# Kernel optimization log

Measured on AMD Instinct MI355X. Metric: run time of the kernel, lower is better.

## Reference

```python
import jax, jax.numpy as jnp
import numpy as np

N, E, HID, HEADS, C, G = 50000, 800000, 64, 4, 64, 64
NEG_SLOPE = 0.2

def _p(key, shape, scale=0.05):
    return jax.random.normal(key, shape, dtype=jnp.float32) * scale

def setup_inputs() -> dict:
    key = jax.random.key(0)
    ks = jax.random.split(key, 24)
    inp = {
        "x": jax.random.normal(ks[0], (N, 6), dtype=jnp.float32),
        "node_type": jax.random.randint(ks[1], (N,), 0, 3, dtype=jnp.int32),
        "edge_index": jax.random.randint(ks[2], (2, E), 0, N, dtype=jnp.int32),
        "edge_attr": jax.random.normal(ks[3], (E, 11), dtype=jnp.float32),
        "batch": jnp.sort(jax.random.randint(ks[4], (N,), 0, G, dtype=jnp.int32)),
        "global_feats": jax.random.normal(ks[5], (G, 6), dtype=jnp.float32),
        # parameters
        "type_emb": _p(ks[6], (3, 4), 1.0),
        "enc_W": _p(ks[7], (10, HID)), "enc_b": jnp.zeros((HID,), jnp.float32),
        "Wl": _p(ks[8], (HID, HEADS * C)), "bl": jnp.zeros((HEADS * C,), jnp.float32),
        "Wr": _p(ks[9], (HID, HEADS * C)), "br": jnp.zeros((HEADS * C,), jnp.float32),
        "We": _p(ks[10], (11, HEADS * C)),
        "att": _p(ks[11], (HEADS, C), 0.1),
        "conv_bias": jnp.zeros((HID,), jnp.float32),
        "gW": _p(ks[12], (6, HID)), "gb": jnp.zeros((HID,), jnp.float32),
        "h1W": _p(ks[13], (2 * HID, HID)), "h1b": jnp.zeros((HID,), jnp.float32),
        "h2W": _p(ks[14], (HID, 1)), "h2b": jnp.zeros((1,), jnp.float32),
    }
    return inp

def reference(x, node_type, edge_index, edge_attr, batch, global_feats,
              type_emb, enc_W, enc_b, Wl, bl, Wr, br, We, att, conv_bias,
              gW, gb, h1W, h1b, h2W, h2b):
    n = x.shape[0]
    g = global_feats.shape[0]
    # node encoder: concat type embedding, linear + relu
    h = jax.nn.relu(jnp.concatenate([x, type_emb[node_type]], axis=1) @ enc_W + enc_b)  # [N, HID]
    # add self-loops with fill_value='mean' edge_attr (PyG default)
    src, dst = edge_index[0], edge_index[1]
    cnt = jax.ops.segment_sum(jnp.ones((edge_attr.shape[0], 1), edge_attr.dtype), dst, num_segments=n)
    loop_attr = jax.ops.segment_sum(edge_attr, dst, num_segments=n) / jnp.maximum(cnt, 1.0)
    loops = jnp.arange(n, dtype=src.dtype)
    src = jnp.concatenate([src, loops]); dst = jnp.concatenate([dst, loops])
    ea = jnp.concatenate([edge_attr, loop_attr], axis=0)  # [E+N, 11]
    # GATv2 transforms
    xl = (h @ Wl + bl).reshape(n, HEADS, C)  # source transform
    xr = (h @ Wr + br).reshape(n, HEADS, C)  # target transform
    ee = (ea @ We).reshape(-1, HEADS, C)     # edge transform
    m = jax.nn.leaky_relu(xl[src] + xr[dst] + ee, NEG_SLOPE)  # [E+N, HEADS, C]
    logits = jnp.einsum('ehc,hc->eh', m, att)  # [E+N, HEADS]
    # segment softmax over incoming edges per target node
    lmax = jax.ops.segment_max(logits, dst, num_segments=n)
    alpha = jnp.exp(logits - lmax[dst])
    denom = jax.ops.segment_sum(alpha, dst, num_segments=n)
    alpha = alpha / (denom[dst] + 1e-16)
    out = jax.ops.segment_sum(alpha[:, :, None] * xl[src], dst, num_segments=n)  # [N, HEADS, C]
    hconv = jax.nn.relu(out.mean(axis=1) + conv_bias)  # concat=False -> mean heads
    # global mean pool over graphs
    gcnt = jax.ops.segment_sum(jnp.ones((n, 1), hconv.dtype), batch, num_segments=g)
    pooled = jax.ops.segment_sum(hconv, batch, num_segments=g) / jnp.maximum(gcnt, 1.0)
    gproj = jax.nn.relu(global_feats @ gW + gb)
    combined = jnp.concatenate([pooled, gproj], axis=1)
    outh = jax.nn.relu(combined @ h1W + h1b) @ h2W + h2b  # dropout inactive (eval)
    return outh.squeeze(1)
```

## Files before the change

### kernel.cpp

```cpp
#include <hip/hip_runtime.h>

#define NEG_SLOPE 0.2f

__device__ __forceinline__ float rl(float v, int l) {
    return __uint_as_float(__builtin_amdgcn_readlane(__float_as_uint(v), l));
}

__global__ void k_deg(const int* __restrict__ dst, int* __restrict__ degi, int E) {
    int e = blockIdx.x * blockDim.x + threadIdx.x;
    if (e >= E) return;
    atomicAdd(&degi[dst[e]], 1);
}

__global__ void __launch_bounds__(1024) k_scan(const int* __restrict__ degi,
                                               int* __restrict__ row_ptr,
                                               int* __restrict__ cursor, int N) {
    __shared__ int wsum[16];
    __shared__ int srun;
    int tid = threadIdx.x, lane = tid & 63, wid = tid >> 6;
    if (tid == 0) srun = 0;
    __syncthreads();
    for (int base = 0; base < N; base += 1024) {
        int i = base + tid;
        int v = (i < N) ? degi[i] : 0;
        int x = v;
#pragma unroll
        for (int off = 1; off < 64; off <<= 1) {
            int y = __shfl_up(x, off, 64);
            if (lane >= off) x += y;
        }
        if (lane == 63) wsum[wid] = x;
        __syncthreads();
        if (wid == 0) {
            int w = (lane < 16) ? wsum[lane] : 0;
#pragma unroll
            for (int off = 1; off < 16; off <<= 1) {
                int y = __shfl_up(w, off, 64);
                if (lane >= off) w += y;
            }
            if (lane < 16) wsum[lane] = w;
        }
        __syncthreads();
        int wofs = (wid > 0) ? wsum[wid - 1] : 0;
        int run = srun;
        if (i < N) {
            int ex = run + wofs + x - v;
            row_ptr[i] = ex;
            cursor[i] = ex;
        }
        __syncthreads();
        if (tid == 1023) srun = run + wsum[15];
        __syncthreads();
    }
    if (tid == 0) row_ptr[N] = srun;
}

__global__ void k_fill(const int* __restrict__ src, const int* __restrict__ dst,
                       int* __restrict__ cursor, int2* __restrict__ csr, int E) {
    int e = blockIdx.x * blockDim.x + threadIdx.x;
    if (e >= E) return;
    int d = dst[e];
    int pos = atomicAdd(&cursor[d], 1);
    csr[pos] = make_int2(src[e], e);
}

__global__ void __launch_bounds__(256) k_enc_xlxr(
    const float* __restrict__ x, const int* __restrict__ node_type,
    const float* __restrict__ type_emb,
    const float* __restrict__ enc_W, const float* __restrict__ enc_b,
    const float* __restrict__ Wl, const float* __restrict__ bl,
    const float* __restrict__ Wr, const float* __restrict__ br,
    float* __restrict__ xl, float* __restrict__ xr, int N) {
    const int NPB = 16;
    __shared__ float sIn[NPB][10];
    __shared__ float sH[NPB][64];
    int tid = threadIdx.x;
    int v0 = blockIdx.x * NPB;
    for (int i = tid; i < NPB * 10; i += 256) {
        int v = i / 10, k = i % 10;
        int vg = v0 + v;
        float val = 0.f;
        if (vg < N) {
            if (k < 6) val = x[(size_t)vg * 6 + k];
            else       val = type_emb[node_type[vg] * 4 + (k - 6)];
        }
        sIn[v][k] = val;
    }
    __syncthreads();
    for (int i = tid; i < NPB * 64; i += 256) {
        int v = i >> 6, j = i & 63;
        float acc = enc_b[j];
#pragma unroll
        for (int k = 0; k < 10; ++k) acc += sIn[v][k] * enc_W[k * 64 + j];
        sH[v][j] = fmaxf(acc, 0.f);
    }
    __syncthreads();
    int j = tid;
    float accL[NPB], accR[NPB];
    float blj = bl[j], brj = br[j];
#pragma unroll
    for (int v = 0; v < NPB; ++v) { accL[v] = blj; accR[v] = brj; }
    for (int k = 0; k < 64; ++k) {
        float wl = Wl[k * 256 + j], wr = Wr[k * 256 + j];
#pragma unroll
        for (int v = 0; v < NPB; ++v) {
            float hv = sH[v][k];
            accL[v] += hv * wl;
            accR[v] += hv * wr;
        }
    }
#pragma unroll
    for (int v = 0; v < NPB; ++v) {
        int vg = v0 + v;
        if (vg < N) {
            xl[(size_t)vg * 256 + j] = accL[v];
            xr[(size_t)vg * 256 + j] = accR[v];
        }
    }
}

__global__ void __launch_bounds__(256, 4) k_gather(
    const int2* __restrict__ csr, const float* __restrict__ edge_attr,
    const int* __restrict__ row_ptr, const float* __restrict__ We,
    const float* __restrict__ att, const float* __restrict__ xl,
    const float* __restrict__ xr, const float* __restrict__ conv_bias,
    const int* __restrict__ batch, float* __restrict__ pooled,
    float* __restrict__ gcnt, int N) {
    int tid = threadIdx.x;
    int lane = tid & 63;
    int h = lane >> 4;
    int c16 = lane & 15;
    int colBase = h * 64 + c16 * 4;
    int v = blockIdx.x * 4 + (tid >> 6);
    if (v >= N) return;

    float rWe[11][4];
#pragma unroll
    for (int k = 0; k < 11; ++k) {
        float4 w = *(const float4*)(We + k * 256 + colBase);
        rWe[k][0] = w.x; rWe[k][1] = w.y; rWe[k][2] = w.z; rWe[k][3] = w.w;
    }
    float4 attv = *(const float4*)(att + colBase);
    float4 xrv  = *(const float4*)(xr + (size_t)v * 256 + colBase);

    float acc0 = 0.f, acc1 = 0.f, acc2 = 0.f, acc3 = 0.f, den = 0.f;
    float ea0 = 0.f, ea1 = 0.f, ea2 = 0.f, ea3 = 0.f;

    int rs = row_ptr[v], re = row_ptr[v + 1];
    int deg = re - rs;
    int attrLaneC = lane / 11; if (attrLaneC > 3) attrLaneC = 3;
    int attrLaneK = lane - attrLaneC * 11;

    for (int base = rs; base < re; base += 64) {
        int cnt = re - base; if (cnt > 64) cnt = 64;
        int cm1 = cnt - 1;
        int2 se = csr[base + ((lane < cnt) ? lane : 0)];
        int myS = se.x, myE = se.y;

        auto LOADB = [&](int t0, float& attrR, float4& x0, float4& x1, float4& x2, float4& x3) {
            int ei = t0 + attrLaneC; if (ei > cm1) ei = cm1;
            int eL = __shfl(myE, ei, 64);
            float a = 0.f;
            if (lane < 44) a = edge_attr[(size_t)eL * 11 + attrLaneK];
            attrR = a;
            int i1 = t0 + 1; if (i1 > cm1) i1 = cm1;
            int i2 = t0 + 2; if (i2 > cm1) i2 = cm1;
            int i3 = t0 + 3; if (i3 > cm1) i3 = cm1;
            int s0 = __builtin_amdgcn_readfirstlane(__shfl(myS, t0, 64));
            int s1 = __builtin_amdgcn_readfirstlane(__shfl(myS, i1, 64));
            int s2 = __builtin_amdgcn_readfirstlane(__shfl(myS, i2, 64));
            int s3 = __builtin_amdgcn_readfirstlane(__shfl(myS, i3, 64));
            x0 = *(const float4*)(xl + (size_t)s0 * 256 + colBase);
            x1 = *(const float4*)(xl + (size_t)s1 * 256 + colBase);
            x2 = *(const float4*)(xl + (size_t)s2 * 256 + colBase);
            x3 = *(const float4*)(xl + (size_t)s3 * 256 + colBase);
        };

        auto EDGE = [&](float attrR, float4 xlv, int cbase) {
            float e0 = 0.f, e1 = 0.f, e2 = 0.f, e3 = 0.f;
#pragma unroll
            for (int k = 0; k < 11; ++k) {
                float s = rl(attrR, cbase + k);
                e0 += s * rWe[k][0]; e1 += s * rWe[k][1];
                e2 += s * rWe[k][2]; e3 += s * rWe[k][3];
            }
            ea0 += e0; ea1 += e1; ea2 += e2; ea3 += e3;
            float m0 = xlv.x + xrv.x + e0;
            float m1 = xlv.y + xrv.y + e1;
            float m2 = xlv.z + xrv.z + e2;
            float m3 = xlv.w + xrv.w + e3;
            m0 = (m0 > 0.f) ? m0 : NEG_SLOPE * m0;
            m1 = (m1 > 0.f) ? m1 : NEG_SLOPE * m1;
            m2 = (m2 > 0.f) ? m2 : NEG_SLOPE * m2;
            m3 = (m3 > 0.f) ? m3 : NEG_SLOPE * m3;
            float t2 = m0 * attv.x + m1 * attv.y + m2 * attv.z + m3 * attv.w;
#pragma unroll
            for (int off = 1; off < 16; off <<= 1) t2 += __shfl_xor(t2, off, 64);
            float p = __expf(t2);
            acc0 += p * xlv.x; acc1 += p * xlv.y; acc2 += p * xlv.z; acc3 += p * xlv.w;
            den += p;
        };

        auto PROC = [&](int t0, float attrR, float4 x0, float4 x1, float4 x2, float4 x3) {
            EDGE(attrR, x0, 0);
            if (t0 + 1 < cnt) EDGE(attrR, x1, 11);
            if (t0 + 2 < cnt) EDGE(attrR, x2, 22);
            if (t0 + 3 < cnt) EDGE(attrR, x3, 33);
        };

        int nb = (cnt + 3) >> 2;
        float attrA, attrB;
        float4 xA0, xA1, xA2, xA3, xB0, xB1, xB2, xB3;
        LOADB(0, attrA, xA0, xA1, xA2, xA3);
        int b = 0;
        while (true) {
            if (b + 1 < nb) LOADB((b + 1) * 4, attrB, xB0, xB1, xB2, xB3);
            PROC(b * 4, attrA, xA0, xA1, xA2, xA3);
            ++b; if (b >= nb) break;
            if (b + 1 < nb) LOADB((b + 1) * 4, attrA, xA0, xA1, xA2, xA3);
            PROC(b * 4, attrB, xB0, xB1, xB2, xB3);
            ++b; if (b >= nb) break;
        }
    }

    {
        float inv = 1.f / fmaxf((float)deg, 1.f);
        float4 xself = *(const float4*)(xl + (size_t)v * 256 + colBase);
        float e0 = ea0 * inv, e1 = ea1 * inv, e2 = ea2 * inv, e3 = ea3 * inv;
        float m0 = xself.x + xrv.x + e0;
        float m1 = xself.y + xrv.y + e1;
        float m2 = xself.z + xrv.z + e2;
        float m3 = xself.w + xrv.w + e3;
        m0 = (m0 > 0.f) ? m0 : NEG_SLOPE * m0;
        m1 = (m1 > 0.f) ? m1 : NEG_SLOPE * m1;
        m2 = (m2 > 0.f) ? m2 : NEG_SLOPE * m2;
        m3 = (m3 > 0.f) ? m3 : NEG_SLOPE * m3;
        float t2 = m0 * attv.x + m1 * attv.y + m2 * attv.z + m3 * attv.w;
#pragma unroll
        for (int off = 1; off < 16; off <<= 1) t2 += __shfl_xor(t2, off, 64);
        float p = __expf(t2);
        acc0 += p * xself.x; acc1 += p * xself.y; acc2 += p * xself.z; acc3 += p * xself.w;
        den += p;
    }

    float r = 1.f / (den + 1e-16f);
    float o0 = acc0 * r, o1 = acc1 * r, o2 = acc2 * r, o3 = acc3 * r;
#pragma unroll
    for (int mask = 16; mask <= 32; mask <<= 1) {
        o0 += __shfl_xor(o0, mask, 64);
        o1 += __shfl_xor(o1, mask, 64);
        o2 += __shfl_xor(o2, mask, 64);
        o3 += __shfl_xor(o3, mask, 64);
    }
    int g = batch[v];
    if (lane < 16) {
        float4 cb = *(const float4*)(conv_bias + c16 * 4);
        float* pg = pooled + g * 64 + c16 * 4;
        atomicAdd(&pg[0], fmaxf(0.25f * o0 + cb.x, 0.f));
        atomicAdd(&pg[1], fmaxf(0.25f * o1 + cb.y, 0.f));
        atomicAdd(&pg[2], fmaxf(0.25f * o2 + cb.z, 0.f));
        atomicAdd(&pg[3], fmaxf(0.25f * o3 + cb.w, 0.f));
    }
    if (lane == 0) atomicAdd(&gcnt[g], 1.0f);
}

__global__ void k_final(const float* __restrict__ pooled, const float* __restrict__ gcnt,
                        const float* __restrict__ gf, const float* __restrict__ gW,
                        const float* __restrict__ gb, const float* __restrict__ h1W,
                        const float* __restrict__ h1b, const float* __restrict__ h2W,
                        const float* __restrict__ h2b, float* __restrict__ out, int G) {
    __shared__ float sComb[128];
    __shared__ float sHid[64];
    int g = blockIdx.x;
    int t = threadIdx.x;
    if (t < 64) {
        sComb[t] = pooled[(size_t)g * 64 + t] / fmaxf(gcnt[g], 1.0f);
    } else {
        int j = t - 64;
        float acc = gb[j];
#pragma unroll
        for (int k = 0; k < 6; ++k) acc += gf[(size_t)g * 6 + k] * gW[k * 64 + j];
        sComb[64 + j] = fmaxf(acc, 0.f);
    }
    __syncthreads();
    if (t < 64) {
        float acc = h1b[t];
#pragma unroll
        for (int k = 0; k < 128; ++k) acc += sComb[k] * h1W[k * 64 + t];
        sHid[t] = fmaxf(acc, 0.f);
    }
    __syncthreads();
    if (t < 64) {
        float p = sHid[t] * h2W[t];
#pragma unroll
        for (int off = 32; off > 0; off >>= 1) p += __shfl_xor(p, off, 64);
        if (t == 0) out[g] = p + h2b[0];
    }
}

extern "C" void kernel_launch(void* const* d_in, const int* in_sizes, int n_in,
                              void* d_out, int out_size, void* d_ws, size_t ws_size,
                              hipStream_t stream) {
    const float* x         = (const float*)d_in[0];
    const int*   node_type = (const int*)d_in[1];
    const int*   edge_index= (const int*)d_in[2];
    const float* edge_attr = (const float*)d_in[3];
    const int*   batch     = (const int*)d_in[4];
    const float* gf        = (const float*)d_in[5];
    const float* type_emb  = (const float*)d_in[6];
    const float* enc_W     = (const float*)d_in[7];
    const float* enc_b     = (const float*)d_in[8];
    const float* Wl        = (const float*)d_in[9];
    const float* bl        = (const float*)d_in[10];
    const float* Wr        = (const float*)d_in[11];
    const float* br        = (const float*)d_in[12];
    const float* We        = (const float*)d_in[13];
    const float* att       = (const float*)d_in[14];
    const float* conv_bias = (const float*)d_in[15];
    const float* gW        = (const float*)d_in[16];
    const float* gb        = (const float*)d_in[17];
    const float* h1W       = (const float*)d_in[18];
    const float* h1b       = (const float*)d_in[19];
    const float* h2W       = (const float*)d_in[20];
    const float* h2b       = (const float*)d_in[21];
    float* out = (float*)d_out;

    const int N = in_sizes[0] / 6;
    const int E = in_sizes[2] / 2;
    const int G = in_sizes[5] / 6;

    const int* srcArr = edge_index;
    const int* dstArr = edge_index + E;

    char* wsb = (char*)d_ws;
    size_t off = 0;
    float* xl      = (float*)(wsb + off); off += (size_t)N * 256 * 4;
    float* xr      = (float*)(wsb + off); off += (size_t)N * 256 * 4;
    int2*  csr     = (int2*) (wsb + off); off += (size_t)E * 8;
    int*   row_ptr = (int*)  (wsb + off); off += (size_t)(N + 1) * 4;
    int*   cursor  = (int*)  (wsb + off); off += (size_t)N * 4;
    size_t zs = off;
    int*   degi    = (int*)  (wsb + off); off += (size_t)N * 4;
    float* pooled  = (float*)(wsb + off); off += (size_t)G * 64 * 4;
    float* gcnt    = (float*)(wsb + off); off += (size_t)G * 4;
    size_t ze = off;
    (void)ws_size; (void)n_in; (void)out_size;

    hipMemsetAsync(wsb + zs, 0, ze - zs, stream);

    k_deg<<<(E + 255) / 256, 256, 0, stream>>>(dstArr, degi, E);
    k_enc_xlxr<<<(N + 15) / 16, 256, 0, stream>>>(x, node_type, type_emb, enc_W, enc_b,
                                                  Wl, bl, Wr, br, xl, xr, N);
    k_scan<<<1, 1024, 0, stream>>>(degi, row_ptr, cursor, N);
    k_fill<<<(E + 255) / 256, 256, 0, stream>>>(srcArr, dstArr, cursor, csr, E);
    k_gather<<<(N + 3) / 4, 256, 0, stream>>>(csr, edge_attr, row_ptr, We, att, xl, xr,
                                              conv_bias, batch, pooled, gcnt, N);
    k_final<<<G, 128, 0, stream>>>(pooled, gcnt, gf, gW, gb, h1W, h1b, h2W, h2b, out, G);
}
```

Baseline: 836.8 us.

## Parallelize CSR scan and batch four-edge processing in gather kernel

Replaces the single-block serial prefix scan with a three-kernel multi-block scan (block-local scan, block-sum scan, offset add), which removes a long single-CU serial loop over all nodes. In the gather kernel, the per-edge attention math is restructured so that four edges are processed together: edge-feature projections, leaky-relu logits and the cross-lane reductions are interleaved for ILP, and invalid edges are masked instead of branched on. Source index extraction switches from shfl+readfirstlane to a direct readlane, and the occupancy hint changes to waves_per_eu(3,4). The four-edge batching raises register pressure and does wasted work on partial groups. The scan adds two kernel launches and only supports up to 64 blocks.

```diff
diff --git a/kernel.cpp b/kernel.cpp
--- a/kernel.cpp
+++ b/kernel.cpp
@@ -12,47 +12,58 @@
     atomicAdd(&degi[dst[e]], 1);
 }
 
-__global__ void __launch_bounds__(1024) k_scan(const int* __restrict__ degi,
-                                               int* __restrict__ row_ptr,
-                                               int* __restrict__ cursor, int N) {
+__global__ void __launch_bounds__(1024) k_scan1(const int* __restrict__ degi,
+                                                int* __restrict__ row_ptr,
+                                                int* __restrict__ bsum, int N) {
     __shared__ int wsum[16];
-    __shared__ int srun;
     int tid = threadIdx.x, lane = tid & 63, wid = tid >> 6;
-    if (tid == 0) srun = 0;
-    __syncthreads();
-    for (int base = 0; base < N; base += 1024) {
-        int i = base + tid;
-        int v = (i < N) ? degi[i] : 0;
-        int x = v;
-#pragma unroll
-        for (int off = 1; off < 64; off <<= 1) {
-            int y = __shfl_up(x, off, 64);
-            if (lane >= off) x += y;
-        }
-        if (lane == 63) wsum[wid] = x;
-        __syncthreads();
-        if (wid == 0) {
-            int w = (lane < 16) ? wsum[lane] : 0;
-#pragma unroll
-            for (int off = 1; off < 16; off <<= 1) {
-                int y = __shfl_up(w, off, 64);
-                if (lane >= off) w += y;
-            }
-            if (lane < 16) wsum[lane] = w;
-        }
-        __syncthreads();
-        int wofs = (wid > 0) ? wsum[wid - 1] : 0;
-        int run = srun;
-        if (i < N) {
-            int ex = run + wofs + x - v;
-            row_ptr[i] = ex;
-            cursor[i] = ex;
-        }
-        __syncthreads();
-        if (tid == 1023) srun = run + wsum[15];
-        __syncthreads();
-    }
-    if (tid == 0) row_ptr[N] = srun;
+    int i = blockIdx.x * 1024 + tid;
+    int v = (i < N) ? degi[i] : 0;
+    int x = v;
+#pragma unroll
+    for (int off = 1; off < 64; off <<= 1) {
+        int y = __shfl_up(x, off, 64);
+        if (lane >= off) x += y;
+    }
+    if (lane == 63) wsum[wid] = x;
+    __syncthreads();
+    if (wid == 0) {
+        int w = (lane < 16) ? wsum[lane] : 0;
+#pragma unroll
+        for (int off = 1; off < 16; off <<= 1) {
+            int y = __shfl_up(w, off, 64);
+            if (lane >= off) w += y;
+        }
+        if (lane < 16) wsum[lane] = w;
+    }
+    __syncthreads();
+    int wofs = (wid > 0) ? wsum[wid - 1] : 0;
+    if (i < N) row_ptr[i] = wofs + x - v;
+    if (tid == 0) bsum[blockIdx.x] = wsum[15];
+}
+
+__global__ void k_scan2(int* __restrict__ bsum, int* __restrict__ row_ptr, int nb, int N) {
+    int lane = threadIdx.x & 63;
+    int v = (lane < nb) ? bsum[lane] : 0;
+    int x = v;
+#pragma unroll
+    for (int off = 1; off < 64; off <<= 1) {
+        int y = __shfl_up(x, off, 64);
+        if (lane >= off) x += y;
+    }
+    if (lane < nb) bsum[lane] = x - v;
+    if (lane == 63) row_ptr[N] = x;
+}
+
+__global__ void __launch_bounds__(1024) k_scan3(int* __restrict__ row_ptr,
+                                                int* __restrict__ cursor,
+                                                const int* __restrict__ bsum, int N) {
+    int i = blockIdx.x * 1024 + threadIdx.x;
+    if (i < N) {
+        int r = row_ptr[i] + bsum[blockIdx.x];
+        row_ptr[i] = r;
+        cursor[i] = r;
+    }
 }
 
 __global__ void k_fill(const int* __restrict__ src, const int* __restrict__ dst,
@@ -119,7 +130,8 @@
     }
 }
 
-__global__ void __launch_bounds__(256, 4) k_gather(
+__global__ void __launch_bounds__(256) __attribute__((amdgpu_waves_per_eu(3, 4)))
+k_gather(
     const int2* __restrict__ csr, const float* __restrict__ edge_attr,
     const int* __restrict__ row_ptr, const float* __restrict__ We,
     const float* __restrict__ att, const float* __restrict__ xl,
@@ -166,46 +178,68 @@
             int i1 = t0 + 1; if (i1 > cm1) i1 = cm1;
             int i2 = t0 + 2; if (i2 > cm1) i2 = cm1;
             int i3 = t0 + 3; if (i3 > cm1) i3 = cm1;
-            int s0 = __builtin_amdgcn_readfirstlane(__shfl(myS, t0, 64));
-            int s1 = __builtin_amdgcn_readfirstlane(__shfl(myS, i1, 64));
-            int s2 = __builtin_amdgcn_readfirstlane(__shfl(myS, i2, 64));
-            int s3 = __builtin_amdgcn_readfirstlane(__shfl(myS, i3, 64));
+            int s0 = __builtin_amdgcn_readlane(myS, t0);
+            int s1 = __builtin_amdgcn_readlane(myS, i1);
+            int s2 = __builtin_amdgcn_readlane(myS, i2);
+            int s3 = __builtin_amdgcn_readlane(myS, i3);
             x0 = *(const float4*)(xl + (size_t)s0 * 256 + colBase);
             x1 = *(const float4*)(xl + (size_t)s1 * 256 + colBase);
             x2 = *(const float4*)(xl + (size_t)s2 * 256 + colBase);
             x3 = *(const float4*)(xl + (size_t)s3 * 256 + colBase);
         };
 
-        auto EDGE = [&](float attrR, float4 xlv, int cbase) {
-            float e0 = 0.f, e1 = 0.f, e2 = 0.f, e3 = 0.f;
+        auto PROC4 = [&](int t0, float attrR, float4 x0, float4 x1, float4 x2, float4 x3) {
+            float p00=0.f,p01=0.f,p02=0.f,p03=0.f;
+            float p10=0.f,p11=0.f,p12=0.f,p13=0.f;
+            float p20=0.f,p21=0.f,p22=0.f,p23=0.f;
+            float p30=0.f,p31=0.f,p32=0.f,p33=0.f;
 #pragma unroll
             for (int k = 0; k < 11; ++k) {
-                float s = rl(attrR, cbase + k);
-                e0 += s * rWe[k][0]; e1 += s * rWe[k][1];
-                e2 += s * rWe[k][2]; e3 += s * rWe[k][3];
+                float w0 = rWe[k][0], w1 = rWe[k][1], w2 = rWe[k][2], w3 = rWe[k][3];
+                float s0 = rl(attrR, k), s1 = rl(attrR, 11 + k);
+                float s2 = rl(attrR, 22 + k), s3 = rl(attrR, 33 + k);
+                p00 += s0*w0; p01 += s0*w1; p02 += s0*w2; p03 += s0*w3;
+                p10 += s1*w0; p11 += s1*w1; p12 += s1*w2; p13 += s1*w3;
+                p20 += s2*w0; p21 += s2*w1; p22 += s2*w2; p23 += s2*w3;
+                p30 += s3*w0; p31 += s3*w1; p32 += s3*w2; p33 += s3*w3;
             }
-            ea0 += e0; ea1 += e1; ea2 += e2; ea3 += e3;
-            float m0 = xlv.x + xrv.x + e0;
-            float m1 = xlv.y + xrv.y + e1;
-            float m2 = xlv.z + xrv.z + e2;
-            float m3 = xlv.w + xrv.w + e3;
-            m0 = (m0 > 0.f) ? m0 : NEG_SLOPE * m0;
-            m1 = (m1 > 0.f) ? m1 : NEG_SLOPE * m1;
-            m2 = (m2 > 0.f) ? m2 : NEG_SLOPE * m2;
-            m3 = (m3 > 0.f) ? m3 : NEG_SLOPE * m3;
-            float t2 = m0 * attv.x + m1 * attv.y + m2 * attv.z + m3 * attv.w;
-#pragma unroll
-            for (int off = 1; off < 16; off <<= 1) t2 += __shfl_xor(t2, off, 64);
-            float p = __expf(t2);
-            acc0 += p * xlv.x; acc1 += p * xlv.y; acc2 += p * xlv.z; acc3 += p * xlv.w;
-            den += p;
-        };
-
-        auto PROC = [&](int t0, float attrR, float4 x0, float4 x1, float4 x2, float4 x3) {
-            EDGE(attrR, x0, 0);
-            if (t0 + 1 < cnt) EDGE(attrR, x1, 11);
-            if (t0 + 2 < cnt) EDGE(attrR, x2, 22);
-            if (t0 + 3 < cnt) EDGE(attrR, x3, 33);
+            bool v1 = (t0 + 1 < cnt), v2 = (t0 + 2 < cnt), v3 = (t0 + 3 < cnt);
+            ea0 += p00 + (v1 ? p10 : 0.f) + (v2 ? p20 : 0.f) + (v3 ? p30 : 0.f);
+            ea1 += p01 + (v1 ? p11 : 0.f) + (v2 ? p21 : 0.f) + (v3 ? p31 : 0.f);
+            ea2 += p02 + (v1 ? p12 : 0.f) + (v2 ? p22 : 0.f) + (v3 ? p32 : 0.f);
+            ea3 += p03 + (v1 ? p13 : 0.f) + (v2 ? p23 : 0.f) + (v3 ? p33 : 0.f);
+            float m, t20, t21, t22, t23;
+            m = x0.x+xrv.x+p00; m=(m>0.f)?m:NEG_SLOPE*m; t20  = m*attv.x;
+            m = x0.y+xrv.y+p01; m=(m>0.f)?m:NEG_SLOPE*m; t20 += m*attv.y;
+            m = x0.z+xrv.z+p02; m=(m>0.f)?m:NEG_SLOPE*m; t20 += m*attv.z;
+            m = x0.w+xrv.w+p03; m=(m>0.f)?m:NEG_SLOPE*m; t20 += m*attv.w;
+            m = x1.x+xrv.x+p10; m=(m>0.f)?m:NEG_SLOPE*m; t21  = m*attv.x;
+            m = x1.y+xrv.y+p11; m=(m>0.f)?m:NEG_SLOPE*m; t21 += m*attv.y;
+            m = x1.z+xrv.z+p12; m=(m>0.f)?m:NEG_SLOPE*m; t21 += m*attv.z;
+            m = x1.w+xrv.w+p13; m=(m>0.f)?m:NEG_SLOPE*m; t21 += m*attv.w;
+            m = x2.x+xrv.x+p20; m=(m>0.f)?m:NEG_SLOPE*m; t22  = m*attv.x;
+            m = x2.y+xrv.y+p21; m=(m>0.f)?m:NEG_SLOPE*m; t22 += m*attv.y;
+            m = x2.z+xrv.z+p22; m=(m>0.f)?m:NEG_SLOPE*m; t22 += m*attv.z;
+            m = x2.w+xrv.w+p23; m=(m>0.f)?m:NEG_SLOPE*m; t22 += m*attv.w;
+            m = x3.x+xrv.x+p30; m=(m>0.f)?m:NEG_SLOPE*m; t23  = m*attv.x;
+            m = x3.y+xrv.y+p31; m=(m>0.f)?m:NEG_SLOPE*m; t23 += m*attv.y;
+            m = x3.z+xrv.z+p32; m=(m>0.f)?m:NEG_SLOPE*m; t23 += m*attv.z;
+            m = x3.w+xrv.w+p33; m=(m>0.f)?m:NEG_SLOPE*m; t23 += m*attv.w;
+#pragma unroll
+            for (int off = 1; off < 16; off <<= 1) {
+                t20 += __shfl_xor(t20, off, 64);
+                t21 += __shfl_xor(t21, off, 64);
+                t22 += __shfl_xor(t22, off, 64);
+                t23 += __shfl_xor(t23, off, 64);
+            }
+            float q0 = __expf(t20), q1 = __expf(t21), q2 = __expf(t22), q3 = __expf(t23);
+            if (!v1) q1 = 0.f;
+            if (!v2) q2 = 0.f;
+            if (!v3) q3 = 0.f;
+            acc0 += q0*x0.x; acc1 += q0*x0.y; acc2 += q0*x0.z; acc3 += q0*x0.w; den += q0;
+            acc0 += q1*x1.x; acc1 += q1*x1.y; acc2 += q1*x1.z; acc3 += q1*x1.w; den += q1;
+            acc0 += q2*x2.x; acc1 += q2*x2.y; acc2 += q2*x2.z; acc3 += q2*x2.w; den += q2;
+            acc0 += q3*x3.x; acc1 += q3*x3.y; acc2 += q3*x3.z; acc3 += q3*x3.w; den += q3;
         };
 
         int nb = (cnt + 3) >> 2;
@@ -215,10 +249,10 @@
         int b = 0;
         while (true) {
             if (b + 1 < nb) LOADB((b + 1) * 4, attrB, xB0, xB1, xB2, xB3);
-            PROC(b * 4, attrA, xA0, xA1, xA2, xA3);
+            PROC4(b * 4, attrA, xA0, xA1, xA2, xA3);
             ++b; if (b >= nb) break;
             if (b + 1 < nb) LOADB((b + 1) * 4, attrA, xA0, xA1, xA2, xA3);
-            PROC(b * 4, attrB, xB0, xB1, xB2, xB3);
+            PROC4(b * 4, attrB, xB0, xB1, xB2, xB3);
             ++b; if (b >= nb) break;
         }
     }
@@ -339,6 +373,7 @@
     int2*  csr     = (int2*) (wsb + off); off += (size_t)E * 8;
     int*   row_ptr = (int*)  (wsb + off); off += (size_t)(N + 1) * 4;
     int*   cursor  = (int*)  (wsb + off); off += (size_t)N * 4;
+    int*   bsum    = (int*)  (wsb + off); off += 64 * 4;
     size_t zs = off;
     int*   degi    = (int*)  (wsb + off); off += (size_t)N * 4;
     float* pooled  = (float*)(wsb + off); off += (size_t)G * 64 * 4;
@@ -348,10 +383,13 @@
 
     hipMemsetAsync(wsb + zs, 0, ze - zs, stream);
 
+    const int nb1 = (N + 1023) / 1024;
     k_deg<<<(E + 255) / 256, 256, 0, stream>>>(dstArr, degi, E);
     k_enc_xlxr<<<(N + 15) / 16, 256, 0, stream>>>(x, node_type, type_emb, enc_W, enc_b,
                                                   Wl, bl, Wr, br, xl, xr, N);
-    k_scan<<<1, 1024, 0, stream>>>(degi, row_ptr, cursor, N);
+    k_scan1<<<nb1, 1024, 0, stream>>>(degi, row_ptr, bsum, N);
+    k_scan2<<<1, 64, 0, stream>>>(bsum, row_ptr, nb1, N);
+    k_scan3<<<nb1, 1024, 0, stream>>>(row_ptr, cursor, bsum, N);
     k_fill<<<(E + 255) / 256, 256, 0, stream>>>(srcArr, dstArr, cursor, csr, E);
     k_gather<<<(N + 3) / 4, 256, 0, stream>>>(csr, edge_attr, row_ptr, We, att, xl, xr,
                                               conv_bias, batch, pooled, gcnt, N);
```

Measured after the change: 781.7 us. -6.6%, faster.
